# Optimization experiments

Hardware: AMD Instinct MI355X
Metric: run time of the kernel (lower is better)

## Reference

```python
import jax, jax.numpy as jnp
from jax import lax
import numpy as np

B, C, L, K = 8, 512, 2048, 3
CQ = C // 8


def setup_inputs() -> dict:
    key = jax.random.key(0)
    k1, k2, k3, k4 = jax.random.split(key, 4)
    scale = 0.05
    return {
        "x": jax.random.normal(k1, (B, C, L), dtype=jnp.float32),
        "Wq": jax.random.normal(k2, (CQ, C, K), dtype=jnp.float32) * scale,
        "Wk": jax.random.normal(k3, (CQ, C, K), dtype=jnp.float32) * scale,
        "Wv": jax.random.normal(k4, (C, C, K), dtype=jnp.float32) * scale,
        "gamma": jnp.ones((1,), dtype=jnp.float32),
    }


def _conv1d(x, w):
    # x: [B, Cin, L], w: [Cout, Cin, K]; 'same' padding = (K-1)//2 on both sides
    pad = (w.shape[-1] - 1) // 2
    return lax.conv_general_dilated(
        x, w, window_strides=(1,), padding=[(pad, pad)],
        dimension_numbers=("NCH", "OIH", "NCH"))


def reference(x, Wq, Wk, Wv, gamma):
    q = _conv1d(x, Wq)  # [B, C/8, L]
    k = _conv1d(x, Wk)  # [B, C/8, L]
    v = _conv1d(x, Wv)  # [B, C, L]
    # scores[b, i, j] = sum_c q[b, c, i] * k[b, c, j]  (q^T k)
    scores = jnp.einsum("bci,bcj->bij", q, k)
    # softmax over dim=1 (the query/i axis) — non-standard axis
    beta = jax.nn.softmax(scores, axis=1)  # [B, L, L]
    out = gamma * jnp.einsum("bcl,blj->bcj", v, beta)  # [B, C, L]
    return out
```

## Files before the change

kernel.cpp:

```cpp
#include <hip/hip_runtime.h>
#include <cstddef>
#include <math.h>

#define L_DIM 2048
#define C_DIM 512
#define CQ_DIM 64
#define B_DIM 8
#define LOG2E 1.44269504088896340736f

typedef _Float16 f16x8 __attribute__((ext_vector_type(8)));
typedef __fp16 fp16x2_t __attribute__((ext_vector_type(2)));
typedef float f32x4 __attribute__((ext_vector_type(4)));

typedef __attribute__((address_space(3))) unsigned int u32_lds;
typedef __attribute__((address_space(1))) const unsigned int u32_glob;

__device__ __forceinline__ unsigned short f2h(float f) {
    union { _Float16 h; unsigned short u; } v;
    v.h = (_Float16)f;
    return v.u;
}

__device__ __forceinline__ unsigned p2u(float a, float b) {
    union { fp16x2_t h; unsigned u; } v;
    v.h = __builtin_amdgcn_cvt_pkrtz(a, b);
    return v.u;
}

__device__ __forceinline__ void gll16(const unsigned short* g, unsigned short* l) {
    __builtin_amdgcn_global_load_lds((u32_glob*)(const void*)g,
                                     (u32_lds*)(void*)l, 16, 0, 0);
}


__global__ __launch_bounds__(256) void prep_w(const float* __restrict__ Wq,
                                              const float* __restrict__ Wk,
                                              const float* __restrict__ Wv,
                                              unsigned short* __restrict__ Wh) {
    const int idx = blockIdx.x * 256 + threadIdx.x;
    const int ci = idx & 511;
    const int co = (idx >> 9) % 640;
    const int t  = idx / (640 * 512);
    float w;
    if (co < 64)       w = Wq[(size_t)co * 1536 + ci * 3 + t];
    else if (co < 128) w = Wk[(size_t)(co - 64) * 1536 + ci * 3 + t];
    else               w = Wv[(size_t)(co - 128) * 1536 + ci * 3 + t];
    Wh[idx] = f2h(w);
}

__global__ __launch_bounds__(256) void prep_x(const float* __restrict__ x,
                                              unsigned short* __restrict__ xT) {
    const int l0  = blockIdx.x * 64;
    const int ci0 = blockIdx.y * 64;
    const int b   = blockIdx.z;

    __shared__ float xs[64][68];
    const int tid = threadIdx.x;
    const float* xb = x + ((size_t)b * C_DIM + ci0) * L_DIM;

    for (int idx = tid; idx < 64 * 16; idx += 256) {
        int ci = idx >> 4, lq = idx & 15;
        *(float4*)&xs[ci][lq * 4] = *(const float4*)&xb[(size_t)ci * L_DIM + l0 + lq * 4];
    }
    __syncthreads();

    unsigned short* ob = xT + ((size_t)b * L_DIM + l0) * C_DIM + ci0;
    for (int idx = tid; idx < 64 * 8; idx += 256) {
        int l = idx >> 3, c8 = idx & 7;
        ushort4 r0, r1;
        r0.x = f2h(xs[c8 * 8 + 0][l]); r0.y = f2h(xs[c8 * 8 + 1][l]);
        r0.z = f2h(xs[c8 * 8 + 2][l]); r0.w = f2h(xs[c8 * 8 + 3][l]);
        r1.x = f2h(xs[c8 * 8 + 4][l]); r1.y = f2h(xs[c8 * 8 + 5][l]);
        r1.z = f2h(xs[c8 * 8 + 6][l]); r1.w = f2h(xs[c8 * 8 + 7][l]);
        *(ushort4*)&ob[(size_t)l * C_DIM + c8 * 8] = r0;
        *(ushort4*)&ob[(size_t)l * C_DIM + c8 * 8 + 4] = r1;
    }
}

__global__ __launch_bounds__(256) void conv_all(const unsigned short* __restrict__ Wh,
                                                const unsigned short* __restrict__ xT,
                                                unsigned short* __restrict__ qT,
                                                unsigned short* __restrict__ kT,
                                                unsigned short* __restrict__ vB) {
    const int l0  = blockIdx.x * 128;
    const int co0 = blockIdx.y * 64;
    const int b   = blockIdx.z;

    __shared__ unsigned short As[3][64][40];
    __shared__ unsigned short Bs[130][40];

    const int tid  = threadIdx.x;
    const int lane = tid & 63, w = tid >> 6;
    const int ln15 = lane & 15, quad = lane >> 4;

    const int co_w = (w & 1) * 32;
    const int l_w  = (w >> 1) * 64;

    const unsigned short* xb = xT + (size_t)b * L_DIM * C_DIM;

    f32x4 acc[2][4] = {};

    for (int ci0 = 0; ci0 < C_DIM; ci0 += 32) {
        __syncthreads();
        for (int idx = tid; idx < 768; idx += 256) {
            int t = idx >> 8, co = (idx >> 2) & 63, c8 = idx & 3;
            *(float4*)&As[t][co][c8 * 8] =
                *(const float4*)&Wh[(((size_t)t * 640) + co0 + co) * C_DIM + ci0 + c8 * 8];
        }
        for (int idx = tid; idx < 520; idx += 256) {
            int la = idx >> 2, c8 = idx & 3;
            int l = l0 - 1 + la;
            float4 vx = {0.f, 0.f, 0.f, 0.f};
            if (l >= 0 && l < L_DIM)
                vx = *(const float4*)&xb[(size_t)l * C_DIM + ci0 + c8 * 8];
            *(float4*)&Bs[la][c8 * 8] = vx;
        }
        __syncthreads();

#pragma unroll
        for (int t = 0; t < 3; t++) {
            f16x8 a[2], bfr[4];
#pragma unroll
            for (int ct = 0; ct < 2; ct++)
                a[ct] = *(const f16x8*)&As[t][co_w + ct * 16 + ln15][quad * 8];
#pragma unroll
            for (int lt = 0; lt < 4; lt++)
                bfr[lt] = *(const f16x8*)&Bs[l_w + lt * 16 + ln15 + t][quad * 8];
#pragma unroll
            for (int ct = 0; ct < 2; ct++)
#pragma unroll
                for (int lt = 0; lt < 4; lt++)
                    acc[ct][lt] = __builtin_amdgcn_mfma_f32_16x16x32_f16(a[ct], bfr[lt], acc[ct][lt], 0, 0, 0);
        }
    }

    if (co0 < 128) {
        const float qs = (co0 == 0) ? LOG2E : 1.0f;
        unsigned short* dst = (co0 == 0 ? qT : kT) + (size_t)b * L_DIM * CQ_DIM;
#pragma unroll
        for (int ct = 0; ct < 2; ct++)
#pragma unroll
            for (int lt = 0; lt < 4; lt++) {
                const int l = l0 + l_w + lt * 16 + ln15;
                const int c = co_w + ct * 16 + quad * 4;
                ushort4 r;
                r.x = f2h(acc[ct][lt][0] * qs); r.y = f2h(acc[ct][lt][1] * qs);
                r.z = f2h(acc[ct][lt][2] * qs); r.w = f2h(acc[ct][lt][3] * qs);
                const size_t off = (size_t)(l >> 4) * 1024 + (c >> 5) * 512
                                 + (((c >> 3) & 3) * 16 + (l & 15)) * 8 + (c & 7);
                *(ushort4*)&dst[off] = r;
            }
    } else {
        unsigned short* dst = vB + (size_t)b * C_DIM * L_DIM;
#pragma unroll
        for (int ct = 0; ct < 2; ct++)
#pragma unroll
            for (int lt = 0; lt < 4; lt++) {
                const int l = l0 + l_w + lt * 16 + ln15;
                const size_t ibase = ((size_t)(l >> 6) * 32) * 1024 + ((l >> 5) & 1) * 512
                                   + (((l >> 3) & 3) * 16) * 8 + (l & 7);
#pragma unroll
                for (int r = 0; r < 4; r++) {
                    const int vco = (co0 - 128) + co_w + ct * 16 + quad * 4 + r;
                    dst[ibase + (size_t)(vco >> 4) * 1024 + (vco & 15) * 8] = f2h(acc[ct][lt][r]);
                }
            }
    }
}

__global__ __launch_bounds__(256) void stat_k(const unsigned short* __restrict__ qT,
                                              const unsigned short* __restrict__ kT,
                                              float* __restrict__ pstat) {
    const int ich = blockIdx.x;
    const int j0  = blockIdx.y * 64;
    const int b   = blockIdx.z;

    const int tid = threadIdx.x;
    const int lane = tid & 63, w = tid >> 6;
    const int ln15 = lane & 15, quad = lane >> 4;
    const int sj = w * 16;
    const int lane8 = lane * 8;

    const unsigned short* qb = qT + (size_t)b * L_DIM * CQ_DIM;
    const unsigned short* kb = kT + (size_t)b * L_DIM * CQ_DIM;

    f16x8 kfr[2];
#pragma unroll
    for (int cc = 0; cc < 2; cc++)
        kfr[cc] = *(const f16x8*)&kb[(size_t)((j0 + sj) >> 4) * 1024 + cc * 512 + lane8];

    float m_run = -1e30f, l_run = 0.f;

    for (int t = 0; t < 4; t++) {
        const int ib = ich * 16 + t * 4;

        f32x4 sacc[4] = {};
#pragma unroll
        for (int cc = 0; cc < 2; cc++) {
#pragma unroll
            for (int it = 0; it < 4; it++) {
                const f16x8 afr = *(const f16x8*)&qb[(size_t)(ib + it) * 1024 + cc * 512 + lane8];
                sacc[it] = __builtin_amdgcn_mfma_f32_16x16x32_f16(afr, kfr[cc], sacc[it], 0, 0, 0);
            }
        }

        float bm = -1e30f;
#pragma unroll
        for (int it = 0; it < 4; it++)
#pragma unroll
            for (int r = 0; r < 4; r++)
                bm = fmaxf(bm, sacc[it][r]);
        bm = fmaxf(bm, __shfl_xor(bm, 16, 64));
        bm = fmaxf(bm, __shfl_xor(bm, 32, 64));
        const float m_new = fmaxf(m_run, bm);
        const float alpha = exp2f(m_run - m_new);

        float lsum = 0.f;
#pragma unroll
        for (int it = 0; it < 4; it++) {
            float p0 = exp2f(sacc[it][0] - m_new);
            float p1 = exp2f(sacc[it][1] - m_new);
            float p2 = exp2f(sacc[it][2] - m_new);
            float p3 = exp2f(sacc[it][3] - m_new);
            lsum += (p0 + p1) + (p2 + p3);
        }
        lsum += __shfl_xor(lsum, 16, 64);
        lsum += __shfl_xor(lsum, 32, 64);
        l_run = l_run * alpha + lsum;
        m_run = m_new;
    }

    if (quad == 0) {
        const int j = j0 + sj + ln15;
        float* pm = pstat;
        float* pl = pstat + 8 * 8 * 2048;
        pm[((size_t)ich * 8 + b) * 2048 + j] = m_run;
        pl[((size_t)ich * 8 + b) * 2048 + j] = l_run;
    }
}

__global__ __launch_bounds__(256) void pv2(const unsigned short* __restrict__ qT,
                                           const unsigned short* __restrict__ kT,
                                           const unsigned short* __restrict__ vB,
                                           const float* __restrict__ pstat,
                                           const float* __restrict__ gamma,
                                           float* __restrict__ out) {
    const int j0  = blockIdx.x * 64;
    const int co0 = blockIdx.y * 128;
    const int b   = blockIdx.z;

    __shared__ __align__(16) unsigned short qbuf[2][4096];
    __shared__ __align__(16) unsigned short vbuf[2][8192];
    __shared__ unsigned short pps[64 * 68];
    __shared__ float mj_s[64];
    __shared__ float il_s[64];

    const int tid = threadIdx.x;
    const int lane = tid & 63, w = tid >> 6;
    const int ln15 = lane & 15, quad = lane >> 4;
    const int lane8 = lane * 8;

    const unsigned short* qb = qT + (size_t)b * L_DIM * CQ_DIM;
    const unsigned short* kb = kT + (size_t)b * L_DIM * CQ_DIM;
    const unsigned short* vb = vB + (size_t)b * C_DIM * L_DIM;

    const int sj  = w * 16;
    const int wco = w * 32;

    {
        const unsigned short* vsrc = vb + (size_t)(co0 >> 4) * 1024;
#pragma unroll
        for (int s = 0; s < 2; s++)
            gll16(qb + (w * 2 + s) * 512 + lane8, &qbuf[0][(w * 2 + s) * 512]);
#pragma unroll
        for (int s = 0; s < 4; s++)
            gll16(vsrc + (w * 4 + s) * 512 + lane8, &vbuf[0][(w * 4 + s) * 512]);
    }

    if (tid < 64) {
        const int j = j0 + tid;
        const float* pm = pstat;
        const float* pl = pstat + 8 * 8 * 2048;
        float m = -1e30f;
        float pmv[8];
#pragma unroll
        for (int c = 0; c < 8; c++) {
            pmv[c] = pm[((size_t)c * 8 + b) * 2048 + j];
            m = fmaxf(m, pmv[c]);
        }
        float l = 0.f;
#pragma unroll
        for (int c = 0; c < 8; c++)
            l = fmaf(pl[((size_t)c * 8 + b) * 2048 + j], exp2f(pmv[c] - m), l);
        mj_s[tid] = m;
        il_s[tid] = gamma[0] / l;
    }

    f16x8 kfr[2];
#pragma unroll
    for (int cc = 0; cc < 2; cc++)
        kfr[cc] = *(const f16x8*)&kb[(size_t)((j0 + sj) >> 4) * 1024 + cc * 512 + lane8];

    __syncthreads();

    const float m_lane = mj_s[sj + ln15];
    float inv[4];
#pragma unroll
    for (int bb = 0; bb < 4; bb++)
        inv[bb] = il_s[bb * 16 + ln15];

    f32x4 oacc[2][4] = {};
    int cur = 0;

    for (int i0 = 0; i0 < L_DIM; i0 += 64) {
        const int i1 = i0 + 64;
        if (i1 < L_DIM) {
            const unsigned short* qsrc = qb + (size_t)(i1 >> 4) * 1024;
            const unsigned short* vsrc = vb + ((size_t)(i1 >> 6) * 32 + (co0 >> 4)) * 1024;
            const int nxt = cur ^ 1;
#pragma unroll
            for (int s = 0; s < 2; s++)
                gll16(qsrc + (w * 2 + s) * 512 + lane8, &qbuf[nxt][(w * 2 + s) * 512]);
#pragma unroll
            for (int s = 0; s < 4; s++)
                gll16(vsrc + (w * 4 + s) * 512 + lane8, &vbuf[nxt][(w * 4 + s) * 512]);
        }

        f32x4 sacc[4] = {};
        __builtin_amdgcn_s_setprio(1);
#pragma unroll
        for (int cc = 0; cc < 2; cc++) {
#pragma unroll
            for (int it = 0; it < 4; it++) {
                const f16x8 afr = *(const f16x8*)&qbuf[cur][(it * 2 + cc) * 512 + lane8];
                sacc[it] = __builtin_amdgcn_mfma_f32_16x16x32_f16(afr, kfr[cc], sacc[it], 0, 0, 0);
            }
        }
        __builtin_amdgcn_s_setprio(0);

        const int j = sj + ln15;
#pragma unroll
        for (int it = 0; it < 4; it++) {
            float p0 = exp2f(sacc[it][0] - m_lane);
            float p1 = exp2f(sacc[it][1] - m_lane);
            float p2 = exp2f(sacc[it][2] - m_lane);
            float p3 = exp2f(sacc[it][3] - m_lane);
            uint2 u;
            u.x = p2u(p0, p1);
            u.y = p2u(p2, p3);
            *(uint2*)&pps[j * 68 + it * 16 + quad * 4] = u;
        }

        asm volatile("s_waitcnt lgkmcnt(0)" ::: "memory");
        __builtin_amdgcn_s_barrier();
        __builtin_amdgcn_sched_barrier(0);

        __builtin_amdgcn_s_setprio(1);
#pragma unroll
        for (int cc = 0; cc < 2; cc++) {
            f16x8 afr[2], bfr[4];
#pragma unroll
            for (int t = 0; t < 2; t++)
                afr[t] = *(const f16x8*)&vbuf[cur][((w * 2 + t) * 2 + cc) * 512 + lane8];
#pragma unroll
            for (int t = 0; t < 4; t++)
                bfr[t] = *(const f16x8*)&pps[(t * 16 + ln15) * 68 + cc * 32 + quad * 8];
#pragma unroll
            for (int a = 0; a < 2; a++)
#pragma unroll
                for (int bb = 0; bb < 4; bb++)
                    oacc[a][bb] = __builtin_amdgcn_mfma_f32_16x16x32_f16(afr[a], bfr[bb], oacc[a][bb], 0, 0, 0);
        }
        __builtin_amdgcn_s_setprio(0);

        __syncthreads();
        cur ^= 1;
    }

#pragma unroll
    for (int a = 0; a < 2; a++)
#pragma unroll
        for (int r = 0; r < 4; r++) {
            const int co = co0 + wco + a * 16 + quad * 4 + r;
            float* ob = out + ((size_t)b * C_DIM + co) * L_DIM + j0;
#pragma unroll
            for (int bb = 0; bb < 4; bb++)
                ob[bb * 16 + ln15] = oacc[a][bb][r] * inv[bb];
        }
}

extern "C" void kernel_launch(void* const* d_in, const int* in_sizes, int n_in,
                              void* d_out, int out_size, void* d_ws, size_t ws_size,
                              hipStream_t stream) {
    const float* x     = (const float*)d_in[0];
    const float* Wq    = (const float*)d_in[1];
    const float* Wk    = (const float*)d_in[2];
    const float* Wv    = (const float*)d_in[3];
    const float* gamma = (const float*)d_in[4];
    float* out = (float*)d_out;

    unsigned short* ws_h = (unsigned short*)d_ws;
    unsigned short* qT = ws_h;
    unsigned short* kT = qT + 1048576;
    unsigned short* vB = kT + 1048576;
    unsigned short* xT = vB + 8388608;
    unsigned short* Wh = xT + 8388608;
    float* pstat = (float*)xT;

    prep_w  <<<3840, 256, 0, stream>>>(Wq, Wk, Wv, Wh);
    prep_x  <<<dim3(32, 8, 8), 256, 0, stream>>>(x, xT);
    conv_all<<<dim3(16, 10, 8), 256, 0, stream>>>(Wh, xT, qT, kT, vB);
    stat_k  <<<dim3(8, 32, 8), 256, 0, stream>>>(qT, kT, pstat);
    pv2     <<<dim3(32, 4, 8), 256, 0, stream>>>(qT, kT, vB, pstat, gamma, out);
}
```

Baseline: 250.2 us.

## Materialize unnormalized softmax probabilities once instead of recomputing per channel block

Adds a kernel that computes the exponentiated scores (using the max over the chunk maxima) once per batch and writes them as an fp16 matrix in an MFMA-friendly tiled layout. A new PV kernel then streams V and this P matrix from global memory instead of recomputing QK^T and exp for each of the four output-channel blocks. This removes redundant score and exp work but adds a 64 MB write and repeated reads of P. The path only runs when the workspace is large enough, and otherwise falls back to the old kernel.

Result: faster. 230.2 us (-8.0%).

```diff
diff --git a/kernel.cpp b/kernel.cpp
--- a/kernel.cpp
+++ b/kernel.cpp
@@ -239,6 +239,173 @@
     }
 }
 
+__global__ __launch_bounds__(256) void sc_p(const unsigned short* __restrict__ qT,
+                                            const unsigned short* __restrict__ kT,
+                                            const float* __restrict__ pstat,
+                                            unsigned short* __restrict__ Pm) {
+    const int ich = blockIdx.x;
+    const int j0  = blockIdx.y * 64;
+    const int b   = blockIdx.z;
+
+    const int tid = threadIdx.x;
+    const int lane = tid & 63, w = tid >> 6;
+    const int ln15 = lane & 15, quad = lane >> 4;
+    const int sj = w * 16;
+    const int lane8 = lane * 8;
+
+    const unsigned short* qb = qT + (size_t)b * L_DIM * CQ_DIM;
+    const unsigned short* kb = kT + (size_t)b * L_DIM * CQ_DIM;
+    unsigned short* Pb = Pm + (size_t)b * L_DIM * L_DIM;
+
+    f16x8 kfr[2];
+#pragma unroll
+    for (int cc = 0; cc < 2; cc++)
+        kfr[cc] = *(const f16x8*)&kb[(size_t)((j0 + sj) >> 4) * 1024 + cc * 512 + lane8];
+
+    const int jl = j0 + sj + ln15;
+    float m = -1e30f;
+#pragma unroll
+    for (int c = 0; c < 8; c++)
+        m = fmaxf(m, pstat[((size_t)c * 8 + b) * 2048 + jl]);
+
+    const int j_tile = (j0 + sj) >> 4;
+    const int inchunk = ((quad >> 1) & 1) * 128 + ln15 * 8 + (quad & 1) * 4;
+
+    for (int t = 0; t < 4; t++) {
+        const int ib = ich * 16 + t * 4;
+
+        f32x4 sacc[4] = {};
+#pragma unroll
+        for (int cc = 0; cc < 2; cc++) {
+#pragma unroll
+            for (int it = 0; it < 4; it++) {
+                const f16x8 afr = *(const f16x8*)&qb[(size_t)(ib + it) * 1024 + cc * 512 + lane8];
+                sacc[it] = __builtin_amdgcn_mfma_f32_16x16x32_f16(afr, kfr[cc], sacc[it], 0, 0, 0);
+            }
+        }
+
+#pragma unroll
+        for (int it = 0; it < 4; it++) {
+            const int i_t32 = ich * 8 + t * 2 + (it >> 1);
+            uint2 u;
+            u.x = p2u(exp2f(sacc[it][0] - m), exp2f(sacc[it][1] - m));
+            u.y = p2u(exp2f(sacc[it][2] - m), exp2f(sacc[it][3] - m));
+            const size_t off = ((size_t)j_tile * 64 + i_t32) * 512
+                             + (((it * 2 + (quad >> 1)) & 3) * 128 + ln15 * 8 + (quad & 1) * 4);
+            *(uint2*)&Pb[off] = u;
+        }
+    }
+}
+
+__global__ __launch_bounds__(256) void pv3(const unsigned short* __restrict__ vB,
+                                           const unsigned short* __restrict__ Pm,
+                                           const float* __restrict__ pstat,
+                                           const float* __restrict__ gamma,
+                                           float* __restrict__ out) {
+    const int j0  = blockIdx.x * 64;
+    const int co0 = blockIdx.y * 128;
+    const int b   = blockIdx.z;
+
+    __shared__ __align__(16) unsigned short vbuf[2][8192];
+    __shared__ __align__(16) unsigned short pbuf[2][4096];
+    __shared__ float il_s[64];
+
+    const int tid = threadIdx.x;
+    const int lane = tid & 63, w = tid >> 6;
+    const int ln15 = lane & 15, quad = lane >> 4;
+    const int lane8 = lane * 8;
+
+    const unsigned short* vb = vB + (size_t)b * C_DIM * L_DIM;
+    const unsigned short* Pb = Pm + (size_t)b * L_DIM * L_DIM;
+
+    {
+        const unsigned short* vsrc = vb + (size_t)(co0 >> 4) * 1024;
+#pragma unroll
+        for (int s = 0; s < 4; s++)
+            gll16(vsrc + (w * 4 + s) * 512 + lane8, &vbuf[0][(w * 4 + s) * 512]);
+#pragma unroll
+        for (int s = 0; s < 2; s++)
+            gll16(Pb + ((size_t)((j0 >> 4) + w) * 64 + s) * 512 + lane8,
+                  &pbuf[0][(w * 2 + s) * 512]);
+    }
+
+    if (tid < 64) {
+        const int j = j0 + tid;
+        const float* pm = pstat;
+        const float* pl = pstat + 8 * 8 * 2048;
+        float m = -1e30f;
+        float pmv[8];
+#pragma unroll
+        for (int c = 0; c < 8; c++) {
+            pmv[c] = pm[((size_t)c * 8 + b) * 2048 + j];
+            m = fmaxf(m, pmv[c]);
+        }
+        float l = 0.f;
+#pragma unroll
+        for (int c = 0; c < 8; c++)
+            l = fmaf(pl[((size_t)c * 8 + b) * 2048 + j], exp2f(pmv[c] - m), l);
+        il_s[tid] = gamma[0] / l;
+    }
+
+    __syncthreads();
+
+    float inv[4];
+#pragma unroll
+    for (int bb = 0; bb < 4; bb++)
+        inv[bb] = il_s[bb * 16 + ln15];
+
+    f32x4 oacc[2][4] = {};
+    int cur = 0;
+
+    for (int i0 = 0; i0 < L_DIM; i0 += 64) {
+        const int i1 = i0 + 64;
+        if (i1 < L_DIM) {
+            const unsigned short* vsrc = vb + ((size_t)(i1 >> 6) * 32 + (co0 >> 4)) * 1024;
+            const int nxt = cur ^ 1;
+#pragma unroll
+            for (int s = 0; s < 4; s++)
+                gll16(vsrc + (w * 4 + s) * 512 + lane8, &vbuf[nxt][(w * 4 + s) * 512]);
+#pragma unroll
+            for (int s = 0; s < 2; s++)
+                gll16(Pb + ((size_t)((j0 >> 4) + w) * 64 + (i1 >> 5) + s) * 512 + lane8,
+                      &pbuf[nxt][(w * 2 + s) * 512]);
+        }
+
+        __builtin_amdgcn_s_setprio(1);
+#pragma unroll
+        for (int cc = 0; cc < 2; cc++) {
+            f16x8 afr[2], bfr[4];
+#pragma unroll
+            for (int t = 0; t < 2; t++)
+                afr[t] = *(const f16x8*)&vbuf[cur][((w * 2 + t) * 2 + cc) * 512 + lane8];
+#pragma unroll
+            for (int t = 0; t < 4; t++)
+                bfr[t] = *(const f16x8*)&pbuf[cur][(t * 2 + cc) * 512 + lane8];
+#pragma unroll
+            for (int a = 0; a < 2; a++)
+#pragma unroll
+                for (int bb = 0; bb < 4; bb++)
+                    oacc[a][bb] = __builtin_amdgcn_mfma_f32_16x16x32_f16(afr[a], bfr[bb], oacc[a][bb], 0, 0, 0);
+        }
+        __builtin_amdgcn_s_setprio(0);
+
+        __syncthreads();
+        cur ^= 1;
+    }
+
+    const int wco = w * 32;
+#pragma unroll
+    for (int a = 0; a < 2; a++)
+#pragma unroll
+        for (int r = 0; r < 4; r++) {
+            const int co = co0 + wco + a * 16 + quad * 4 + r;
+            float* ob = out + ((size_t)b * C_DIM + co) * L_DIM + j0;
+#pragma unroll
+            for (int bb = 0; bb < 4; bb++)
+                ob[bb * 16 + ln15] = oacc[a][bb][r] * inv[bb];
+        }
+}
+
 __global__ __launch_bounds__(256) void pv2(const unsigned short* __restrict__ qT,
                                            const unsigned short* __restrict__ kT,
                                            const unsigned short* __restrict__ vB,
@@ -405,11 +572,19 @@
     unsigned short* vB = kT + 1048576;
     unsigned short* xT = vB + 8388608;
     unsigned short* Wh = xT + 8388608;
+    unsigned short* Pm = Wh + 983040;
     float* pstat = (float*)xT;
+
+    const size_t need_bytes = ((size_t)19857408 + 33554432) * 2;
 
     prep_w  <<<3840, 256, 0, stream>>>(Wq, Wk, Wv, Wh);
     prep_x  <<<dim3(32, 8, 8), 256, 0, stream>>>(x, xT);
     conv_all<<<dim3(16, 10, 8), 256, 0, stream>>>(Wh, xT, qT, kT, vB);
     stat_k  <<<dim3(8, 32, 8), 256, 0, stream>>>(qT, kT, pstat);
-    pv2     <<<dim3(32, 4, 8), 256, 0, stream>>>(qT, kT, vB, pstat, gamma, out);
-}
+    if (ws_size >= need_bytes) {
+        sc_p <<<dim3(8, 32, 8), 256, 0, stream>>>(qT, kT, pstat, Pm);
+        pv3  <<<dim3(32, 4, 8), 256, 0, stream>>>(vB, Pm, pstat, gamma, out);
+    } else {
+        pv2  <<<dim3(32, 4, 8), 256, 0, stream>>>(qT, kT, vB, pstat, gamma, out);
+    }
+}
```
